# Performance work log

Hardware: AMD Instinct MI355X
Metric: run time of the kernel (lower is better)

## Reference

```python
import jax, jax.numpy as jnp
import numpy as np

# --- static config (matches init_kwargs) ---
B = 2; HI = 60; WI = 60; T = 4; WS = 8; SHIFT = 4
C = 256; NH = 8; HD = C // NH; HID = 1024
P = HI * WI; N = T * P
PAD = (WS - HI % WS) % WS           # 4 -> pad 60 -> 64
HP = HI + PAD; WP = WI + PAD
NWH = HP // WS; NWW = WP // WS
L = WS * WS                          # 64 tokens per window
SCALE = HD ** -0.5

# relative position index [L, L] (constant)
_c = np.stack(np.meshgrid(np.arange(WS), np.arange(WS), indexing='ij')).reshape(2, -1)
_r = (_c[:, :, None] - _c[:, None, :]).transpose(1, 2, 0) + WS - 1
REL_IDX = jnp.asarray(_r[..., 0] * (2 * WS - 1) + _r[..., 1])

# per-window key padding mask [nWin, L] (True = padded token)
_b = np.zeros((HP, WP), bool); _b[HI:, :] = True; _b[:, WI:] = True
WIN_MASK = jnp.asarray(_b.reshape(NWH, WS, NWW, WS).transpose(0, 2, 1, 3).reshape(NWH * NWW, L))


def _ln(x, w, b):
    m = x.mean(-1, keepdims=True)
    v = jnp.square(x - m).mean(-1, keepdims=True)
    return (x - m) * jax.lax.rsqrt(v + 1e-5) * w + b


def _partition(x4):  # [Bm, HP, WP, C] -> [Bm*nWin, L, C]
    Bm = x4.shape[0]
    return x4.reshape(Bm, NWH, WS, NWW, WS, C).transpose(0, 1, 3, 2, 4, 5).reshape(Bm * NWH * NWW, L, C)


def _win_attn(xq, xkv, qw, qb, kw, kb, vw, vb, ow, ob, bias_table):
    Bm = B * T
    q4 = xq.reshape(Bm, HI, WI, C)
    k4 = xkv.reshape(Bm, HI, WI, C)
    q4 = jnp.roll(q4, (-SHIFT, -SHIFT), (1, 2))
    k4 = jnp.roll(k4, (-SHIFT, -SHIFT), (1, 2))
    pad = ((0, 0), (0, PAD), (0, PAD), (0, 0))
    q4 = jnp.pad(q4, pad); k4 = jnp.pad(k4, pad)
    q_win = _partition(q4)   # [Bw, L, C]
    kv_win = _partition(k4)
    q = (q_win @ qw.T + qb).reshape(-1, L, NH, HD)
    k = (kv_win @ kw.T + kb).reshape(-1, L, NH, HD)
    v = (kv_win @ vw.T + vb).reshape(-1, L, NH, HD)
    attn = jnp.einsum('bihd,bjhd->bhij', q, k) * SCALE
    attn = attn + bias_table[REL_IDX].transpose(2, 0, 1)[None]      # RPB [1,H,L,L]
    km = jnp.tile(WIN_MASK, (Bm, 1))                                  # [Bw, L]
    attn = jnp.where(km[:, None, None, :], -jnp.inf, attn)
    p = jax.nn.softmax(attn, axis=-1)
    o = jnp.einsum('bhij,bjhd->bihd', p, v).reshape(-1, L, C)
    o = o @ ow.T + ob
    y = o.reshape(Bm, NWH, NWW, WS, WS, C).transpose(0, 1, 3, 2, 4, 5).reshape(Bm, HP, WP, C)
    y = y[:, :HI, :WI, :]
    y = jnp.roll(y, (SHIFT, SHIFT), (1, 2))
    return y.reshape(B, N, C)


def reference(x, context, ln1_w, ln1_b, ln2_w, ln2_b, ln3_w, ln3_b, lnc_w, lnc_b,
              sa_q_w, sa_q_b, sa_k_w, sa_k_b, sa_v_w, sa_v_b, sa_o_w, sa_o_b, sa_bias,
              ca_q_w, ca_q_b, ca_k_w, ca_k_b, ca_v_w, ca_v_b, ca_o_w, ca_o_b, ca_bias,
              gamma1, gamma2, gamma_mlp, mlp_w1, mlp_b1, mlp_w2, mlp_b2):
    xn = _ln(x, ln1_w, ln1_b)
    y_s = _win_attn(xn, xn, sa_q_w, sa_q_b, sa_k_w, sa_k_b, sa_v_w, sa_v_b, sa_o_w, sa_o_b, sa_bias)
    x = x + gamma1 * y_s
    y_c = _win_attn(_ln(x, ln2_w, ln2_b), _ln(context, lnc_w, lnc_b),
                    ca_q_w, ca_q_b, ca_k_w, ca_k_b, ca_v_w, ca_v_b, ca_o_w, ca_o_b, ca_bias)
    x = x + gamma2 * y_c
    h = _ln(x, ln3_w, ln3_b)
    h = jax.nn.gelu(h @ mlp_w1.T + mlp_b1, approximate=False) @ mlp_w2.T + mlp_b2
    return x + gamma_mlp * h


def setup_inputs() -> dict:
    key = jax.random.key(0)
    ks = jax.random.split(key, 16)
    def w(k, shape, s=0.02):
        return jax.random.normal(k, shape, jnp.float32) * s
    inp = {}
    inp['x'] = jax.random.normal(ks[0], (B, N, C), jnp.float32)
    inp['context'] = jax.random.normal(ks[1], (B, N, C), jnp.float32)
    for nm in ['ln1', 'ln2', 'ln3', 'lnc']:
        inp[f'{nm}_w'] = jnp.ones((C,), jnp.float32)
        inp[f'{nm}_b'] = jnp.zeros((C,), jnp.float32)
    i = 2
    for pfx in ['sa', 'ca']:
        for pn in ['q', 'k', 'v', 'o']:
            inp[f'{pfx}_{pn}_w'] = w(ks[i], (C, C)); i += 1
            inp[f'{pfx}_{pn}_b'] = jnp.zeros((C,), jnp.float32)
        inp[f'{pfx}_bias'] = w(ks[i], ((2 * WS - 1) * (2 * WS - 1), NH)); i += 1
    inp['gamma1'] = jnp.ones((1,), jnp.float32)
    inp['gamma2'] = jnp.ones((1,), jnp.float32)
    inp['gamma_mlp'] = jnp.full((1,), 0.1, jnp.float32)
    inp['mlp_w1'] = w(ks[i], (HID, C)); i += 1
    inp['mlp_b1'] = jnp.zeros((HID,), jnp.float32)
    inp['mlp_w2'] = w(ks[i], (C, HID)); i += 1
    inp['mlp_b2'] = jnp.zeros((C,), jnp.float32)
    return inp
```

## Files before the change

kernel.cpp:

```cpp
#include <hip/hip_runtime.h>
#include <math.h>

#define BN    28800
#define CC    256
#define HIDN  1024
#define WINS  512
#define WROWS (WINS*64)
#define ATT_SCALE 0.1767766952966369f

typedef __bf16 bf16x8 __attribute__((ext_vector_type(8)));
typedef float  f32x4  __attribute__((ext_vector_type(4)));

__device__ __forceinline__ unsigned short f2bf(float f) {
    unsigned u = __float_as_uint(f);
    unsigned r = (u + 0x7FFFu + ((u >> 16) & 1u)) >> 16;
    return (unsigned short)r;
}
__device__ __forceinline__ float bf2f(unsigned short u) {
    return __uint_as_float((unsigned)u << 16);
}

__device__ __forceinline__ float gelu_f(float x) {
    float x3 = x * x * x;
    float e  = __expf(1.5957691216057308f * (x + 0.044715f * x3));
    float th = 1.0f - 2.0f * __builtin_amdgcn_rcpf(e + 1.0f);
    return 0.5f * x * (1.0f + th);
}

__device__ __forceinline__ void gl_lds16(const void* g, void* l) {
    __builtin_amdgcn_global_load_lds(
        (const __attribute__((address_space(1))) void*)g,
        (__attribute__((address_space(3))) void*)l, 16, 0, 0);
}

__global__ void ln_kernel(const float* __restrict__ x, const float* __restrict__ w,
                          const float* __restrict__ b, unsigned short* __restrict__ out, int ntok) {
    int tok  = (int)((blockIdx.x * blockDim.x + threadIdx.x) >> 6);
    int lane = threadIdx.x & 63;
    if (tok >= ntok) return;
    float4 v = reinterpret_cast<const float4*>(x + (size_t)tok * CC)[lane];
    float s  = v.x + v.y + v.z + v.w;
    float s2 = v.x*v.x + v.y*v.y + v.z*v.z + v.w*v.w;
#pragma unroll
    for (int off = 32; off >= 1; off >>= 1) {
        s  += __shfl_xor(s, off);
        s2 += __shfl_xor(s2, off);
    }
    float mean = s * (1.0f / CC);
    float var  = s2 * (1.0f / CC) - mean * mean;
    float rs   = rsqrtf(var + 1e-5f);
    float4 wv = reinterpret_cast<const float4*>(w)[lane];
    float4 bv = reinterpret_cast<const float4*>(b)[lane];
    ushort4 o;
    o.x = f2bf((v.x - mean) * rs * wv.x + bv.x);
    o.y = f2bf((v.y - mean) * rs * wv.y + bv.y);
    o.z = f2bf((v.z - mean) * rs * wv.z + bv.z);
    o.w = f2bf((v.w - mean) * rs * wv.w + bv.w);
    reinterpret_cast<ushort4*>(out + (size_t)tok * CC)[lane] = o;
}

__global__ void ln_gather(const float* __restrict__ x, const float* __restrict__ w,
                          const float* __restrict__ b, unsigned short* __restrict__ dst) {
    int row  = (int)((blockIdx.x * blockDim.x + threadIdx.x) >> 6);
    int lane = threadIdx.x & 63;
    if (row >= WROWS) return;
    int win = row >> 6, l = row & 63;
    int f   = win >> 6;
    int wih = (win >> 3) & 7, wiw = win & 7;
    int r = l >> 3, s = l & 7;
    int h = wih * 8 + r, wc = wiw * 8 + s;
    if (h >= 60 || wc >= 60) {
        ushort4 z = {0, 0, 0, 0};
        reinterpret_cast<ushort4*>(dst + (size_t)row * CC)[lane] = z;
        return;
    }
    int oh = (h + 4) % 60, ow = (wc + 4) % 60;
    size_t tok = (size_t)f * 3600 + (size_t)oh * 60 + ow;
    float4 v = reinterpret_cast<const float4*>(x + tok * CC)[lane];
    float sm  = v.x + v.y + v.z + v.w;
    float s2 = v.x*v.x + v.y*v.y + v.z*v.z + v.w*v.w;
#pragma unroll
    for (int off = 32; off >= 1; off >>= 1) {
        sm += __shfl_xor(sm, off);
        s2 += __shfl_xor(s2, off);
    }
    float mean = sm * (1.0f / CC);
    float var  = s2 * (1.0f / CC) - mean * mean;
    float rs   = rsqrtf(var + 1e-5f);
    float4 wv = reinterpret_cast<const float4*>(w)[lane];
    float4 bv = reinterpret_cast<const float4*>(b)[lane];
    ushort4 o;
    o.x = f2bf((v.x - mean) * rs * wv.x + bv.x);
    o.y = f2bf((v.y - mean) * rs * wv.y + bv.y);
    o.z = f2bf((v.z - mean) * rs * wv.z + bv.z);
    o.w = f2bf((v.w - mean) * rs * wv.w + bv.w);
    reinterpret_cast<ushort4*>(dst + (size_t)row * CC)[lane] = o;
}

template <bool GELU, int FUSE, int TN>
__global__ __launch_bounds__(512, 4) void gemm_wa(
        const unsigned short* __restrict__ Wt,
        const unsigned short* __restrict__ Act,
        const float* __restrict__ b0, const float* __restrict__ b1,
        const float* __restrict__ b2, const float* __restrict__ b3,
        unsigned short* __restrict__ o0, unsigned short* __restrict__ o1,
        unsigned short* __restrict__ o2, unsigned short* __restrict__ o3,
        int strideO, int vseg, int K, int Ntok,
        const float* __restrict__ xres, const float* __restrict__ gammap,
        float* __restrict__ fout) {
    constexpr int NW   = TN / 64;
    constexpr int BP   = TN / 128;
    constexpr int BUFB = 8192 + TN * 64;
    constexpr int POOLB = (3 * BUFB > TN * 256) ? 3 * BUFB : TN * 256;
    __shared__ __align__(16) char pool[POOLB];
    unsigned short* Cs = (unsigned short*)pool;

    const int t = threadIdx.x;
    const int w = t >> 6;
    const int l = t & 63;
    const int Mb = gridDim.x;
    int lin = blockIdx.y * Mb + blockIdx.x;
    int T = Mb * gridDim.y;
    int q = T >> 3, rr = T & 7;
    int xcd = lin & 7, slot = lin >> 3;
    int wid = (xcd < rr) ? (xcd * (q + 1) + slot)
                         : (rr * (q + 1) + (xcd - rr) * q + slot);
    const int m0 = (wid % Mb) * 128;
    const int n0 = (wid / Mb) * TN;

    const int wr = w >> 2, wc = w & 3;
    const int r = l & 15, g = l >> 4;
    const int gp = (g ^ ((r >> 1) & 3)) * 8;
    const int srow = t >> 2;
    const int sgl  = (t & 3) ^ ((srow >> 1) & 3);

    f32x4 acc[4][NW];
#pragma unroll
    for (int i = 0; i < 4; ++i)
#pragma unroll
        for (int j = 0; j < NW; ++j) { acc[i][j][0]=0.f; acc[i][j][1]=0.f; acc[i][j][2]=0.f; acc[i][j][3]=0.f; }

#define STAGE(k0, buf)                                                             \
    do {                                                                           \
        gl_lds16(Wt + (size_t)(m0 + srow) * K + (k0) + sgl * 8,                    \
                 pool + (buf) * BUFB + w * 1024);                                  \
        _Pragma("unroll")                                                          \
        for (int p = 0; p < BP; ++p) {                                             \
            int c    = p * 512 + t;                                                \
            int rowb = c >> 2;                                                     \
            int glb  = (c & 3) ^ ((rowb >> 1) & 3);                                \
            gl_lds16(Act + (size_t)(n0 + rowb) * K + (k0) + glb * 8,               \
                     pool + (buf) * BUFB + 8192 + p * 8192 + w * 1024);            \
        }                                                                          \
    } while (0)

    STAGE(0, 0);
    STAGE(32, 1);
    const char* cb0 = pool;
    const char* cb1 = pool + BUFB;
    const char* cb2 = pool + 2 * BUFB;
    int sbuf = 2;
    const int nt = K >> 5;
    for (int kt = 0; kt < nt; ++kt) {
        if (kt < nt - 1) {
            if (TN == 128) asm volatile("s_waitcnt vmcnt(2)" ::: "memory");
            else           asm volatile("s_waitcnt vmcnt(3)" ::: "memory");
        } else {
            asm volatile("s_waitcnt vmcnt(0)" ::: "memory");
        }
        __builtin_amdgcn_s_barrier();
        __builtin_amdgcn_sched_barrier(0);
        const unsigned short* cA = (const unsigned short*)cb0;
        const unsigned short* cB = (const unsigned short*)(cb0 + 8192);
        bf16x8 bw[NW];
#pragma unroll
        for (int n = 0; n < NW; ++n)
            bw[n] = *reinterpret_cast<const bf16x8*>(&cB[(wc * (NW * 16) + n * 16 + r) * 32 + gp]);
        __builtin_amdgcn_s_setprio(1);
#pragma unroll
        for (int m = 0; m < 4; ++m) {
            bf16x8 af = *reinterpret_cast<const bf16x8*>(&cA[(wr * 64 + m * 16 + r) * 32 + gp]);
#pragma unroll
            for (int n = 0; n < NW; ++n)
                acc[m][n] = __builtin_amdgcn_mfma_f32_16x16x32_bf16(af, bw[n], acc[m][n], 0, 0, 0);
        }
        __builtin_amdgcn_s_setprio(0);
        if (kt + 2 < nt) {
            STAGE((kt + 2) * 32, sbuf);
            sbuf = (sbuf == 2) ? 0 : sbuf + 1;
        }
        const char* tmp = cb0; cb0 = cb1; cb1 = cb2; cb2 = tmp;
    }
#undef STAGE

    const int seg = m0 >> 8;
    const float* bp = (seg == 0) ? b0 : (seg == 1) ? b1 : (seg == 2) ? b2 : b3;
    unsigned short* op = (seg == 0) ? o0 : (seg == 1) ? o1 : (seg == 2) ? o2 : o3;
    const int chseg = m0 & 255;

    if (FUSE == 0 && seg == vseg) {
#pragma unroll
        for (int m = 0; m < 4; ++m) {
            const int ch0 = chseg + wr * 64 + m * 16 + g * 4;
            float4 b4 = *reinterpret_cast<const float4*>(bp + ch0);
            const float bb[4] = {b4.x, b4.y, b4.z, b4.w};
#pragma unroll
            for (int n = 0; n < NW; ++n) {
                const int tok = n0 + wc * (NW * 16) + n * 16 + r;
#pragma unroll
                for (int j = 0; j < 4; ++j)
                    op[(size_t)(ch0 + j) * 32768 + tok] = f2bf(acc[m][n][j] + bb[j]);
            }
        }
        return;
    }

    __syncthreads();
#pragma unroll
    for (int m = 0; m < 4; ++m) {
        const int ch0 = wr * 64 + m * 16 + g * 4;
        float4 b4 = *reinterpret_cast<const float4*>(bp + chseg + ch0);
        const float bb[4] = {b4.x, b4.y, b4.z, b4.w};
#pragma unroll
        for (int n = 0; n < NW; ++n) {
            const int tok_l = wc * (NW * 16) + n * 16 + r;
            float cv[4];
#pragma unroll
            for (int j = 0; j < 4; ++j) {
                cv[j] = acc[m][n][j] + bb[j];
                if (GELU) cv[j] = gelu_f(cv[j]);
            }
            ushort4 pk;
            pk.x = f2bf(cv[0]); pk.y = f2bf(cv[1]); pk.z = f2bf(cv[2]); pk.w = f2bf(cv[3]);
            int gran = (ch0 >> 2) ^ ((tok_l & 15) << 1);
            reinterpret_cast<ushort4*>(Cs)[tok_l * 32 + gran] = pk;
        }
    }
    __syncthreads();
    const int u = t & 15, trow = t >> 4;
    if (FUSE == 0) {
#pragma unroll
        for (int it = 0; it < TN / 32; ++it) {
            int tok_l = it * 32 + trow;
            if (n0 + tok_l >= Ntok) continue;
            int up = u ^ (tok_l & 15);
            uint4 v = reinterpret_cast<const uint4*>(Cs)[tok_l * 16 + up];
            *reinterpret_cast<uint4*>(op + (size_t)(n0 + tok_l) * strideO + chseg + u * 8) = v;
        }
    } else {
        const float gsc = gammap[0];
#pragma unroll
        for (int it = 0; it < TN / 32; ++it) {
            int tok_l = it * 32 + trow;
            int wrow = n0 + tok_l;
            if (wrow >= Ntok) continue;
            int tok;
            if (FUSE == 1) {
                int win = wrow >> 6, l2 = wrow & 63;
                int f = win >> 6, wih = (win >> 3) & 7, wiw = win & 7;
                int r2 = l2 >> 3, s2 = l2 & 7;
                int h = wih * 8 + r2, wcol = wiw * 8 + s2;
                if (h >= 60 || wcol >= 60) continue;
                int oh = h + 4; if (oh >= 60) oh -= 60;
                int ow = wcol + 4; if (ow >= 60) ow -= 60;
                tok = f * 3600 + oh * 60 + ow;
            } else {
                tok = wrow;
            }
            int up = u ^ (tok_l & 15);
            uint4 v = reinterpret_cast<const uint4*>(Cs)[tok_l * 16 + up];
            const unsigned short* pu = (const unsigned short*)&v;
            const float* xr = xres + (size_t)tok * CC + chseg + u * 8;
            float4 xa = *reinterpret_cast<const float4*>(xr);
            float4 xb = *reinterpret_cast<const float4*>(xr + 4);
            float4 oa, ob;
            oa.x = xa.x + gsc * bf2f(pu[0]);
            oa.y = xa.y + gsc * bf2f(pu[1]);
            oa.z = xa.z + gsc * bf2f(pu[2]);
            oa.w = xa.w + gsc * bf2f(pu[3]);
            ob.x = xb.x + gsc * bf2f(pu[4]);
            ob.y = xb.y + gsc * bf2f(pu[5]);
            ob.z = xb.z + gsc * bf2f(pu[6]);
            ob.w = xb.w + gsc * bf2f(pu[7]);
            float* fo = fout + (size_t)tok * CC + chseg + u * 8;
            *reinterpret_cast<float4*>(fo) = oa;
            *reinterpret_cast<float4*>(fo + 4) = ob;
        }
    }
}

__global__ void expand_bias(const float* __restrict__ sa, const float* __restrict__ ca,
                            float* __restrict__ dst) {
    int e = (int)(blockIdx.x * blockDim.x + threadIdx.x);
    const float* src = (e < 16384) ? sa : ca;
    int e2 = e & 16383;
    int h = e2 >> 12, ij = e2 & 4095, i = ij >> 6, j = ij & 63;
    int ri = i >> 3, si = i & 7, rj = j >> 3, sj = j & 7;
    dst[e] = src[((ri - rj + 7) * 15 + (si - sj + 7)) * 8 + h];
}

__global__ __launch_bounds__(256) void attn_mfma(
        const unsigned short* __restrict__ Q,
        const unsigned short* __restrict__ K,
        const unsigned short* __restrict__ VT,
        const float* __restrict__ biasx,
        unsigned short* __restrict__ AO) {
    __shared__ __align__(16) unsigned short Pl[4][64 * 64];
    const int t = threadIdx.x;
    const int w = t >> 6, l = t & 63;
    const int win = blockIdx.x >> 1;
    const int h   = (blockIdx.x & 1) * 4 + w;
    const int c = l & 15, g = l >> 4;
    const int wih = (win >> 3) & 7, wiw = win & 7;
    const size_t qkbase = (size_t)win * 64 * CC + (size_t)h * 32;

    bf16x8 ka[4], qb[4];
#pragma unroll
    for (int mj = 0; mj < 4; ++mj)
        ka[mj] = *reinterpret_cast<const bf16x8*>(K + qkbase + (size_t)(mj * 16 + c) * CC + g * 8);
#pragma unroll
    for (int ni = 0; ni < 4; ++ni)
        qb[ni] = *reinterpret_cast<const bf16x8*>(Q + qkbase + (size_t)(ni * 16 + c) * CC + g * 8);
    f32x4 s[4][4];
#pragma unroll
    for (int mj = 0; mj < 4; ++mj)
#pragma unroll
        for (int ni = 0; ni < 4; ++ni) { s[mj][ni][0]=0.f; s[mj][ni][1]=0.f; s[mj][ni][2]=0.f; s[mj][ni][3]=0.f; }
#pragma unroll
    for (int mj = 0; mj < 4; ++mj)
#pragma unroll
        for (int ni = 0; ni < 4; ++ni)
            s[mj][ni] = __builtin_amdgcn_mfma_f32_16x16x32_bf16(ka[mj], qb[ni], s[mj][ni], 0, 0, 0);

    const float* bx = biasx + h * 4096;
    const bool modd = (wiw == 7) && (g & 1);
#pragma unroll
    for (int mj = 0; mj < 4; ++mj) {
        const bool mmj = (wih == 7) && (mj >= 2);
#pragma unroll
        for (int ni = 0; ni < 4; ++ni) {
            float4 b4 = *reinterpret_cast<const float4*>(bx + (ni * 16 + c) * 64 + mj * 16 + g * 4);
            const float bb[4] = {b4.x, b4.y, b4.z, b4.w};
#pragma unroll
            for (int jj = 0; jj < 4; ++jj) {
                float v = s[mj][ni][jj] * ATT_SCALE + bb[jj];
                s[mj][ni][jj] = (mmj || modd) ? -1e30f : v;
            }
        }
    }

#pragma unroll
    for (int ni = 0; ni < 4; ++ni) {
        float mx = -1e30f;
#pragma unroll
        for (int mj = 0; mj < 4; ++mj)
#pragma unroll
            for (int jj = 0; jj < 4; ++jj) mx = fmaxf(mx, s[mj][ni][jj]);
        mx = fmaxf(mx, __shfl_xor(mx, 16));
        mx = fmaxf(mx, __shfl_xor(mx, 32));
        float sum = 0.f;
#pragma unroll
        for (int mj = 0; mj < 4; ++mj)
#pragma unroll
            for (int jj = 0; jj < 4; ++jj) {
                float p = __expf(s[mj][ni][jj] - mx);
                s[mj][ni][jj] = p;
                sum += p;
            }
        sum += __shfl_xor(sum, 16);
        sum += __shfl_xor(sum, 32);
        float rinv = __builtin_amdgcn_rcpf(sum);
        const int i  = ni * 16 + c;
        const int ik = i & 7;
#pragma unroll
        for (int mj = 0; mj < 4; ++mj) {
            ushort4 pk;
            pk.x = f2bf(s[mj][ni][0] * rinv);
            pk.y = f2bf(s[mj][ni][1] * rinv);
            pk.z = f2bf(s[mj][ni][2] * rinv);
            pk.w = f2bf(s[mj][ni][3] * rinv);
            int chunk = (mj * 2 + (g >> 1)) ^ ik;
            *reinterpret_cast<ushort4*>((char*)&Pl[w][0] + i * 128 + chunk * 16 + (g & 1) * 8) = pk;
        }
    }

    bf16x8 vb[2][2];
#pragma unroll
    for (int nd = 0; nd < 2; ++nd)
#pragma unroll
        for (int kt = 0; kt < 2; ++kt)
            vb[nd][kt] = *reinterpret_cast<const bf16x8*>(
                VT + (size_t)(h * 32 + nd * 16 + c) * 32768 + win * 64 + kt * 32 + g * 8);
    f32x4 o[4][2];
#pragma unroll
    for (int mi = 0; mi < 4; ++mi)
#pragma unroll
        for (int nd = 0; nd < 2; ++nd) { o[mi][nd][0]=0.f; o[mi][nd][1]=0.f; o[mi][nd][2]=0.f; o[mi][nd][3]=0.f; }
#pragma unroll
    for (int mi = 0; mi < 4; ++mi) {
        const int i  = mi * 16 + c;
        const int ik = i & 7;
#pragma unroll
        for (int kt = 0; kt < 2; ++kt) {
            int chunk = (kt * 4 + g) ^ ik;
            bf16x8 pa = *reinterpret_cast<const bf16x8*>((char*)&Pl[w][0] + i * 128 + chunk * 16);
#pragma unroll
            for (int nd = 0; nd < 2; ++nd)
                o[mi][nd] = __builtin_amdgcn_mfma_f32_16x16x32_bf16(pa, vb[nd][kt], o[mi][nd], 0, 0, 0);
        }
    }

    unsigned short* aop = AO + qkbase;
#pragma unroll
    for (int mi = 0; mi < 4; ++mi)
#pragma unroll
        for (int nd = 0; nd < 2; ++nd)
#pragma unroll
            for (int jj = 0; jj < 4; ++jj)
                aop[(size_t)(mi * 16 + g * 4 + jj) * CC + nd * 16 + c] = f2bf(o[mi][nd][jj]);
}

__global__ void cvt_all(const float* s0, const float* s1, const float* s2, const float* s3,
                        const float* s4, const float* s5, const float* s6, const float* s7,
                        const float* s8, const float* s9, unsigned short* __restrict__ dst) {
    const float* srcs[10] = {s0, s1, s2, s3, s4, s5, s6, s7, s8, s9};
    int blk = blockIdx.x;
    int wi = (blk < 512) ? (blk >> 6) : (blk < 768 ? 8 : 9);
    size_t start = (wi < 8) ? (size_t)wi * 65536 : (wi == 8 ? (size_t)524288 : (size_t)786432);
    size_t gidx = (size_t)blk * 1024 + (size_t)threadIdx.x * 4;
    float4 v = *reinterpret_cast<const float4*>(srcs[wi] + (gidx - start));
    ushort4 o;
    o.x = f2bf(v.x); o.y = f2bf(v.y); o.z = f2bf(v.z); o.w = f2bf(v.w);
    *reinterpret_cast<ushort4*>(dst + gidx) = o;
}

extern "C" void kernel_launch(void* const* d_in, const int* in_sizes, int n_in,
                              void* d_out, int out_size, void* d_ws, size_t ws_size,
                              hipStream_t stream) {
    const float* x    = (const float*)d_in[0];
    const float* ctx  = (const float*)d_in[1];
    const float* ln1w = (const float*)d_in[2];
    const float* ln1b = (const float*)d_in[3];
    const float* ln2w = (const float*)d_in[4];
    const float* ln2b = (const float*)d_in[5];
    const float* ln3w = (const float*)d_in[6];
    const float* ln3b = (const float*)d_in[7];
    const float* lncw = (const float*)d_in[8];
    const float* lncb = (const float*)d_in[9];
    const float* saqw = (const float*)d_in[10];
    const float* saqb = (const float*)d_in[11];
    const float* sakw = (const float*)d_in[12];
    const float* sakb = (const float*)d_in[13];
    const float* savw = (const float*)d_in[14];
    const float* savb = (const float*)d_in[15];
    const float* saow = (const float*)d_in[16];
    const float* saob = (const float*)d_in[17];
    const float* sabias = (const float*)d_in[18];
    const float* caqw = (const float*)d_in[19];
    const float* caqb = (const float*)d_in[20];
    const float* cakw = (const float*)d_in[21];
    const float* cakb = (const float*)d_in[22];
    const float* cavw = (const float*)d_in[23];
    const float* cavb = (const float*)d_in[24];
    const float* caow = (const float*)d_in[25];
    const float* caob = (const float*)d_in[26];
    const float* cabias = (const float*)d_in[27];
    const float* gamma1 = (const float*)d_in[28];
    const float* gamma2 = (const float*)d_in[29];
    const float* gammam = (const float*)d_in[30];
    const float* mw1 = (const float*)d_in[31];
    const float* mb1 = (const float*)d_in[32];
    const float* mw2 = (const float*)d_in[33];
    const float* mb2 = (const float*)d_in[34];

    float* ws = (float*)d_ws;
    unsigned short* LNbf = (unsigned short*)(ws);
    unsigned short* Gq   = (unsigned short*)(ws + 3686400);
    unsigned short* Gkv  = (unsigned short*)(ws + 7880704);
    unsigned short* Qbf  = (unsigned short*)(ws + 12075008);
    unsigned short* Kbf  = (unsigned short*)(ws + 16269312);
    unsigned short* VTbf = (unsigned short*)(ws + 20463616);
    float* X1  = ws + 28852224;
    unsigned short* Wp = (unsigned short*)(ws + 36225024);
    float* biasx = ws + 36749312;
    unsigned short* AObf = Gq;
    unsigned short* H1bf = Qbf;

    unsigned short* w_saqkv = Wp;
    unsigned short* w_sao   = Wp + 196608;
    unsigned short* w_caq   = Wp + 262144;
    unsigned short* w_cakv  = Wp + 327680;
    unsigned short* w_cao   = Wp + 458752;
    unsigned short* w_m1    = Wp + 524288;
    unsigned short* w_m2    = Wp + 786432;

    float* OUT = (float*)d_out;

    dim3 blk(256);
    dim3 blk512(512);
    dim3 gLN(BN / 4);
    dim3 gGather(WROWS / 4);
    dim3 gAttn(WINS * 2);

    cvt_all<<<dim3(1024), blk, 0, stream>>>(saqw, sakw, savw, saow, caqw, cakw, cavw, caow, mw1, mw2, Wp);
    expand_bias<<<dim3(128), blk, 0, stream>>>(sabias, cabias, biasx);

    ln_gather<<<gGather, blk, 0, stream>>>(x, ln1w, ln1b, Gq);
    gemm_wa<false,0,256><<<dim3(6, 128), blk512, 0, stream>>>(w_saqkv, Gq, saqb, sakb, savb, savb,
                                                              Qbf, Kbf, VTbf, VTbf, CC, 2, CC, WROWS,
                                                              nullptr, nullptr, nullptr);
    attn_mfma<<<gAttn, blk, 0, stream>>>(Qbf, Kbf, VTbf, biasx, AObf);
    gemm_wa<false,1,128><<<dim3(2, 256), blk512, 0, stream>>>(w_sao, AObf, saob, saob, saob, saob,
                                                              Qbf, Qbf, Qbf, Qbf, CC, -1, CC, WROWS,
                                                              x, gamma1, X1);
    ln_gather<<<gGather, blk, 0, stream>>>(X1, ln2w, ln2b, Gq);
    ln_gather<<<gGather, blk, 0, stream>>>(ctx, lncw, lncb, Gkv);
    gemm_wa<false,0,128><<<dim3(2, 256), blk512, 0, stream>>>(w_caq, Gq, caqb, caqb, caqb, caqb,
                                                              Qbf, Qbf, Qbf, Qbf, CC, -1, CC, WROWS,
                                                              nullptr, nullptr, nullptr);
    gemm_wa<false,0,256><<<dim3(4, 128), blk512, 0, stream>>>(w_cakv, Gkv, cakb, cavb, cavb, cavb,
                                                              Kbf, VTbf, VTbf, VTbf, CC, 1, CC, WROWS,
                                                              nullptr, nullptr, nullptr);
    attn_mfma<<<gAttn, blk, 0, stream>>>(Qbf, Kbf, VTbf, biasx + 16384, AObf);
    gemm_wa<false,1,128><<<dim3(2, 256), blk512, 0, stream>>>(w_cao, AObf, caob, caob, caob, caob,
                                                              Qbf, Qbf, Qbf, Qbf, CC, -1, CC, WROWS,
                                                              X1, gamma2, X1);
    ln_kernel<<<gLN, blk, 0, stream>>>(X1, ln3w, ln3b, LNbf, BN);
    gemm_wa<true,0,256><<<dim3(8, 113), blk512, 0, stream>>>(w_m1, LNbf, mb1, mb1 + 256, mb1 + 512, mb1 + 768,
                                                             H1bf, H1bf + 256, H1bf + 512, H1bf + 768,
                                                             HIDN, -1, CC, BN, nullptr, nullptr, nullptr);
    gemm_wa<false,2,256><<<dim3(2, 113), blk512, 0, stream>>>(w_m2, H1bf, mb2, mb2, mb2, mb2,
                                                             Qbf, Qbf, Qbf, Qbf, CC, -1, HIDN, BN,
                                                             X1, gammam, OUT);
}
```

Baseline: 239.5 us.

## Enlarge GEMM output-channel tile to 256 and stage the epilogue in halves

The weight-activation GEMM now covers 256 output channels per block instead of 128. Each wave accumulates 8x NW MFMA tiles, and twice the weight rows are staged per k-step, so every activation tile loaded from global memory is reused across all channels of a segment. The epilogue writes through LDS in 128-token halves so the C staging buffer fits the pool. Grids are halved in the channel dimension, and the MLP2 GEMM switches to a 128-token tile. The cost is much higher register pressure (launch bounds drop to 2 blocks per SM for TN=256) and larger shared memory, which reduces occupancy.

```diff
diff --git a/kernel.cpp b/kernel.cpp
--- a/kernel.cpp
+++ b/kernel.cpp
@@ -98,7 +98,7 @@
 }
 
 template <bool GELU, int FUSE, int TN>
-__global__ __launch_bounds__(512, 4) void gemm_wa(
+__global__ __launch_bounds__(512, (TN == 128) ? 4 : 2) void gemm_wa(
         const unsigned short* __restrict__ Wt,
         const unsigned short* __restrict__ Act,
         const float* __restrict__ b0, const float* __restrict__ b1,
@@ -110,8 +110,9 @@
         float* __restrict__ fout) {
     constexpr int NW   = TN / 64;
     constexpr int BP   = TN / 128;
-    constexpr int BUFB = 8192 + TN * 64;
-    constexpr int POOLB = (3 * BUFB > TN * 256) ? 3 * BUFB : TN * 256;
+    constexpr int BUFB = 16384 + TN * 64;
+    constexpr int HALVES = TN / 128;
+    constexpr int POOLB = (3 * BUFB > 65536) ? 3 * BUFB : 65536;
     __shared__ __align__(16) char pool[POOLB];
     unsigned short* Cs = (unsigned short*)pool;
 
@@ -125,32 +126,37 @@
     int xcd = lin & 7, slot = lin >> 3;
     int wid = (xcd < rr) ? (xcd * (q + 1) + slot)
                          : (rr * (q + 1) + (xcd - rr) * q + slot);
-    const int m0 = (wid % Mb) * 128;
+    const int m0 = (wid % Mb) * 256;
     const int n0 = (wid / Mb) * TN;
 
-    const int wr = w >> 2, wc = w & 3;
+    const int wr = w >> 2;
+    const int wc = w & 3;
     const int r = l & 15, g = l >> 4;
     const int gp = (g ^ ((r >> 1) & 3)) * 8;
-    const int srow = t >> 2;
-    const int sgl  = (t & 3) ^ ((srow >> 1) & 3);
-
-    f32x4 acc[4][NW];
-#pragma unroll
-    for (int i = 0; i < 4; ++i)
+
+    f32x4 acc[8][NW];
+#pragma unroll
+    for (int i = 0; i < 8; ++i)
 #pragma unroll
         for (int j = 0; j < NW; ++j) { acc[i][j][0]=0.f; acc[i][j][1]=0.f; acc[i][j][2]=0.f; acc[i][j][3]=0.f; }
 
 #define STAGE(k0, buf)                                                             \
     do {                                                                           \
-        gl_lds16(Wt + (size_t)(m0 + srow) * K + (k0) + sgl * 8,                    \
-                 pool + (buf) * BUFB + w * 1024);                                  \
+        _Pragma("unroll")                                                          \
+        for (int p = 0; p < 2; ++p) {                                              \
+            int c    = p * 512 + t;                                                \
+            int rowa = c >> 2;                                                     \
+            int gla  = (c & 3) ^ ((rowa >> 1) & 3);                                \
+            gl_lds16(Wt + (size_t)(m0 + rowa) * K + (k0) + gla * 8,                \
+                     pool + (buf) * BUFB + (p * 512 + w * 64) * 16);               \
+        }                                                                          \
         _Pragma("unroll")                                                          \
         for (int p = 0; p < BP; ++p) {                                             \
             int c    = p * 512 + t;                                                \
             int rowb = c >> 2;                                                     \
             int glb  = (c & 3) ^ ((rowb >> 1) & 3);                                \
             gl_lds16(Act + (size_t)(n0 + rowb) * K + (k0) + glb * 8,               \
-                     pool + (buf) * BUFB + 8192 + p * 8192 + w * 1024);            \
+                     pool + (buf) * BUFB + 16384 + (p * 512 + w * 64) * 16);       \
         }                                                                          \
     } while (0)
 
@@ -163,23 +169,23 @@
     const int nt = K >> 5;
     for (int kt = 0; kt < nt; ++kt) {
         if (kt < nt - 1) {
-            if (TN == 128) asm volatile("s_waitcnt vmcnt(2)" ::: "memory");
-            else           asm volatile("s_waitcnt vmcnt(3)" ::: "memory");
+            if (TN == 128) asm volatile("s_waitcnt vmcnt(3)" ::: "memory");
+            else           asm volatile("s_waitcnt vmcnt(4)" ::: "memory");
         } else {
             asm volatile("s_waitcnt vmcnt(0)" ::: "memory");
         }
         __builtin_amdgcn_s_barrier();
         __builtin_amdgcn_sched_barrier(0);
         const unsigned short* cA = (const unsigned short*)cb0;
-        const unsigned short* cB = (const unsigned short*)(cb0 + 8192);
+        const unsigned short* cB = (const unsigned short*)(cb0 + 16384);
         bf16x8 bw[NW];
 #pragma unroll
         for (int n = 0; n < NW; ++n)
             bw[n] = *reinterpret_cast<const bf16x8*>(&cB[(wc * (NW * 16) + n * 16 + r) * 32 + gp]);
         __builtin_amdgcn_s_setprio(1);
 #pragma unroll
-        for (int m = 0; m < 4; ++m) {
-            bf16x8 af = *reinterpret_cast<const bf16x8*>(&cA[(wr * 64 + m * 16 + r) * 32 + gp]);
+        for (int m = 0; m < 8; ++m) {
+            bf16x8 af = *reinterpret_cast<const bf16x8*>(&cA[(wr * 128 + m * 16 + r) * 32 + gp]);
 #pragma unroll
             for (int n = 0; n < NW; ++n)
                 acc[m][n] = __builtin_amdgcn_mfma_f32_16x16x32_bf16(af, bw[n], acc[m][n], 0, 0, 0);
@@ -196,12 +202,11 @@
     const int seg = m0 >> 8;
     const float* bp = (seg == 0) ? b0 : (seg == 1) ? b1 : (seg == 2) ? b2 : b3;
     unsigned short* op = (seg == 0) ? o0 : (seg == 1) ? o1 : (seg == 2) ? o2 : o3;
-    const int chseg = m0 & 255;
 
     if (FUSE == 0 && seg == vseg) {
 #pragma unroll
-        for (int m = 0; m < 4; ++m) {
-            const int ch0 = chseg + wr * 64 + m * 16 + g * 4;
+        for (int m = 0; m < 8; ++m) {
+            const int ch0 = wr * 128 + m * 16 + g * 4;
             float4 b4 = *reinterpret_cast<const float4*>(bp + ch0);
             const float bb[4] = {b4.x, b4.y, b4.z, b4.w};
 #pragma unroll
@@ -215,76 +220,74 @@
         return;
     }
 
-    __syncthreads();
-#pragma unroll
-    for (int m = 0; m < 4; ++m) {
-        const int ch0 = wr * 64 + m * 16 + g * 4;
-        float4 b4 = *reinterpret_cast<const float4*>(bp + chseg + ch0);
-        const float bb[4] = {b4.x, b4.y, b4.z, b4.w};
-#pragma unroll
-        for (int n = 0; n < NW; ++n) {
-            const int tok_l = wc * (NW * 16) + n * 16 + r;
-            float cv[4];
-#pragma unroll
-            for (int j = 0; j < 4; ++j) {
-                cv[j] = acc[m][n][j] + bb[j];
-                if (GELU) cv[j] = gelu_f(cv[j]);
+    const float gsc = (FUSE != 0) ? gammap[0] : 0.f;
+    const int u16 = t & 31, trow = t >> 5;
+#pragma unroll
+    for (int h = 0; h < HALVES; ++h) {
+        __syncthreads();
+        if (HALVES == 1 || (wc >> 1) == h) {
+#pragma unroll
+            for (int m = 0; m < 8; ++m) {
+                const int ch0 = wr * 128 + m * 16 + g * 4;
+                float4 b4 = *reinterpret_cast<const float4*>(bp + ch0);
+                const float bb[4] = {b4.x, b4.y, b4.z, b4.w};
+#pragma unroll
+                for (int n = 0; n < NW; ++n) {
+                    const int tokh = (wc * (NW * 16) + n * 16 + r) & 127;
+                    float cv[4];
+#pragma unroll
+                    for (int j = 0; j < 4; ++j) {
+                        cv[j] = acc[m][n][j] + bb[j];
+                        if (GELU) cv[j] = gelu_f(cv[j]);
+                    }
+                    ushort4 pk;
+                    pk.x = f2bf(cv[0]); pk.y = f2bf(cv[1]); pk.z = f2bf(cv[2]); pk.w = f2bf(cv[3]);
+                    int gran = (ch0 >> 2) ^ ((tokh & 15) << 1);
+                    reinterpret_cast<ushort4*>(Cs)[tokh * 64 + gran] = pk;
+                }
             }
-            ushort4 pk;
-            pk.x = f2bf(cv[0]); pk.y = f2bf(cv[1]); pk.z = f2bf(cv[2]); pk.w = f2bf(cv[3]);
-            int gran = (ch0 >> 2) ^ ((tok_l & 15) << 1);
-            reinterpret_cast<ushort4*>(Cs)[tok_l * 32 + gran] = pk;
-        }
-    }
-    __syncthreads();
-    const int u = t & 15, trow = t >> 4;
-    if (FUSE == 0) {
-#pragma unroll
-        for (int it = 0; it < TN / 32; ++it) {
-            int tok_l = it * 32 + trow;
-            if (n0 + tok_l >= Ntok) continue;
-            int up = u ^ (tok_l & 15);
-            uint4 v = reinterpret_cast<const uint4*>(Cs)[tok_l * 16 + up];
-            *reinterpret_cast<uint4*>(op + (size_t)(n0 + tok_l) * strideO + chseg + u * 8) = v;
-        }
-    } else {
-        const float gsc = gammap[0];
-#pragma unroll
-        for (int it = 0; it < TN / 32; ++it) {
-            int tok_l = it * 32 + trow;
-            int wrow = n0 + tok_l;
+        }
+        __syncthreads();
+#pragma unroll
+        for (int it = 0; it < 8; ++it) {
+            int rowh = it * 16 + trow;
+            int wrow = n0 + h * 128 + rowh;
             if (wrow >= Ntok) continue;
-            int tok;
-            if (FUSE == 1) {
-                int win = wrow >> 6, l2 = wrow & 63;
-                int f = win >> 6, wih = (win >> 3) & 7, wiw = win & 7;
-                int r2 = l2 >> 3, s2 = l2 & 7;
-                int h = wih * 8 + r2, wcol = wiw * 8 + s2;
-                if (h >= 60 || wcol >= 60) continue;
-                int oh = h + 4; if (oh >= 60) oh -= 60;
-                int ow = wcol + 4; if (ow >= 60) ow -= 60;
-                tok = f * 3600 + oh * 60 + ow;
+            int up = u16 ^ (rowh & 15);
+            uint4 v = reinterpret_cast<const uint4*>(Cs)[rowh * 32 + up];
+            if (FUSE == 0) {
+                *reinterpret_cast<uint4*>(op + (size_t)wrow * strideO + u16 * 8) = v;
             } else {
-                tok = wrow;
+                int tok;
+                if (FUSE == 1) {
+                    int win = wrow >> 6, l2 = wrow & 63;
+                    int f = win >> 6, wih = (win >> 3) & 7, wiw = win & 7;
+                    int r2 = l2 >> 3, s2 = l2 & 7;
+                    int hh = wih * 8 + r2, wcol = wiw * 8 + s2;
+                    if (hh >= 60 || wcol >= 60) continue;
+                    int oh = hh + 4; if (oh >= 60) oh -= 60;
+                    int ow = wcol + 4; if (ow >= 60) ow -= 60;
+                    tok = f * 3600 + oh * 60 + ow;
+                } else {
+                    tok = wrow;
+                }
+                const unsigned short* pu = (const unsigned short*)&v;
+                const float* xr = xres + (size_t)tok * CC + u16 * 8;
+                float4 xa = *reinterpret_cast<const float4*>(xr);
+                float4 xb = *reinterpret_cast<const float4*>(xr + 4);
+                float4 oa, ob;
+                oa.x = xa.x + gsc * bf2f(pu[0]);
+                oa.y = xa.y + gsc * bf2f(pu[1]);
+                oa.z = xa.z + gsc * bf2f(pu[2]);
+                oa.w = xa.w + gsc * bf2f(pu[3]);
+                ob.x = xb.x + gsc * bf2f(pu[4]);
+                ob.y = xb.y + gsc * bf2f(pu[5]);
+                ob.z = xb.z + gsc * bf2f(pu[6]);
+                ob.w = xb.w + gsc * bf2f(pu[7]);
+                float* fo = fout + (size_t)tok * CC + u16 * 8;
+                *reinterpret_cast<float4*>(fo) = oa;
+                *reinterpret_cast<float4*>(fo + 4) = ob;
             }
-            int up = u ^ (tok_l & 15);
-            uint4 v = reinterpret_cast<const uint4*>(Cs)[tok_l * 16 + up];
-            const unsigned short* pu = (const unsigned short*)&v;
-            const float* xr = xres + (size_t)tok * CC + chseg + u * 8;
-            float4 xa = *reinterpret_cast<const float4*>(xr);
-            float4 xb = *reinterpret_cast<const float4*>(xr + 4);
-            float4 oa, ob;
-            oa.x = xa.x + gsc * bf2f(pu[0]);
-            oa.y = xa.y + gsc * bf2f(pu[1]);
-            oa.z = xa.z + gsc * bf2f(pu[2]);
-            oa.w = xa.w + gsc * bf2f(pu[3]);
-            ob.x = xb.x + gsc * bf2f(pu[4]);
-            ob.y = xb.y + gsc * bf2f(pu[5]);
-            ob.z = xb.z + gsc * bf2f(pu[6]);
-            ob.w = xb.w + gsc * bf2f(pu[7]);
-            float* fo = fout + (size_t)tok * CC + chseg + u * 8;
-            *reinterpret_cast<float4*>(fo) = oa;
-            *reinterpret_cast<float4*>(fo + 4) = ob;
         }
     }
 }
@@ -506,30 +509,30 @@
     expand_bias<<<dim3(128), blk, 0, stream>>>(sabias, cabias, biasx);
 
     ln_gather<<<gGather, blk, 0, stream>>>(x, ln1w, ln1b, Gq);
-    gemm_wa<false,0,256><<<dim3(6, 128), blk512, 0, stream>>>(w_saqkv, Gq, saqb, sakb, savb, savb,
+    gemm_wa<false,0,256><<<dim3(3, 128), blk512, 0, stream>>>(w_saqkv, Gq, saqb, sakb, savb, savb,
                                                               Qbf, Kbf, VTbf, VTbf, CC, 2, CC, WROWS,
                                                               nullptr, nullptr, nullptr);
     attn_mfma<<<gAttn, blk, 0, stream>>>(Qbf, Kbf, VTbf, biasx, AObf);
-    gemm_wa<false,1,128><<<dim3(2, 256), blk512, 0, stream>>>(w_sao, AObf, saob, saob, saob, saob,
+    gemm_wa<false,1,128><<<dim3(1, 256), blk512, 0, stream>>>(w_sao, AObf, saob, saob, saob, saob,
                                                               Qbf, Qbf, Qbf, Qbf, CC, -1, CC, WROWS,
                                                               x, gamma1, X1);
     ln_gather<<<gGather, blk, 0, stream>>>(X1, ln2w, ln2b, Gq);
     ln_gather<<<gGather, blk, 0, stream>>>(ctx, lncw, lncb, Gkv);
-    gemm_wa<false,0,128><<<dim3(2, 256), blk512, 0, stream>>>(w_caq, Gq, caqb, caqb, caqb, caqb,
+    gemm_wa<false,0,128><<<dim3(1, 256), blk512, 0, stream>>>(w_caq, Gq, caqb, caqb, caqb, caqb,
                                                               Qbf, Qbf, Qbf, Qbf, CC, -1, CC, WROWS,
                                                               nullptr, nullptr, nullptr);
-    gemm_wa<false,0,256><<<dim3(4, 128), blk512, 0, stream>>>(w_cakv, Gkv, cakb, cavb, cavb, cavb,
+    gemm_wa<false,0,256><<<dim3(2, 128), blk512, 0, stream>>>(w_cakv, Gkv, cakb, cavb, cavb, cavb,
                                                               Kbf, VTbf, VTbf, VTbf, CC, 1, CC, WROWS,
                                                               nullptr, nullptr, nullptr);
     attn_mfma<<<gAttn, blk, 0, stream>>>(Qbf, Kbf, VTbf, biasx + 16384, AObf);
-    gemm_wa<false,1,128><<<dim3(2, 256), blk512, 0, stream>>>(w_cao, AObf, caob, caob, caob, caob,
+    gemm_wa<false,1,128><<<dim3(1, 256), blk512, 0, stream>>>(w_cao, AObf, caob, caob, caob, caob,
                                                               Qbf, Qbf, Qbf, Qbf, CC, -1, CC, WROWS,
                                                               X1, gamma2, X1);
     ln_kernel<<<gLN, blk, 0, stream>>>(X1, ln3w, ln3b, LNbf, BN);
-    gemm_wa<true,0,256><<<dim3(8, 113), blk512, 0, stream>>>(w_m1, LNbf, mb1, mb1 + 256, mb1 + 512, mb1 + 768,
+    gemm_wa<true,0,256><<<dim3(4, 113), blk512, 0, stream>>>(w_m1, LNbf, mb1, mb1 + 256, mb1 + 512, mb1 + 768,
                                                              H1bf, H1bf + 256, H1bf + 512, H1bf + 768,
                                                              HIDN, -1, CC, BN, nullptr, nullptr, nullptr);
-    gemm_wa<false,2,256><<<dim3(2, 113), blk512, 0, stream>>>(w_m2, H1bf, mb2, mb2, mb2, mb2,
+    gemm_wa<false,2,128><<<dim3(1, 225), blk512, 0, stream>>>(w_m2, H1bf, mb2, mb2, mb2, mb2,
                                                              Qbf, Qbf, Qbf, Qbf, CC, -1, HIDN, BN,
                                                              X1, gammam, OUT);
 }
```

Measured after the change: 263.9 us. +10.2%, slower.

## Fuse output projection, residual add and following LayerNorm into one GEMM kernel

Applied to the files above, without the earlier changes.

Adds a gemm_ln kernel that computes the full 256-channel output projection per 128-token tile, so each block holds whole rows and can apply the residual add and the next LayerNorm in its epilogue. This replaces the separate ln_gather after self-attention and the ln_kernel after cross-attention, removing a full re-read of the fp32 residual stream and two launches. The cost is a larger per-block tile with fewer blocks (256), which may lower parallelism. AObf is moved to its own buffer so the fused kernel can write Gq while reading the attention output.

```diff
diff --git a/kernel.cpp b/kernel.cpp
--- a/kernel.cpp
+++ b/kernel.cpp
@@ -31,32 +31,6 @@
     __builtin_amdgcn_global_load_lds(
         (const __attribute__((address_space(1))) void*)g,
         (__attribute__((address_space(3))) void*)l, 16, 0, 0);
-}
-
-__global__ void ln_kernel(const float* __restrict__ x, const float* __restrict__ w,
-                          const float* __restrict__ b, unsigned short* __restrict__ out, int ntok) {
-    int tok  = (int)((blockIdx.x * blockDim.x + threadIdx.x) >> 6);
-    int lane = threadIdx.x & 63;
-    if (tok >= ntok) return;
-    float4 v = reinterpret_cast<const float4*>(x + (size_t)tok * CC)[lane];
-    float s  = v.x + v.y + v.z + v.w;
-    float s2 = v.x*v.x + v.y*v.y + v.z*v.z + v.w*v.w;
-#pragma unroll
-    for (int off = 32; off >= 1; off >>= 1) {
-        s  += __shfl_xor(s, off);
-        s2 += __shfl_xor(s2, off);
-    }
-    float mean = s * (1.0f / CC);
-    float var  = s2 * (1.0f / CC) - mean * mean;
-    float rs   = rsqrtf(var + 1e-5f);
-    float4 wv = reinterpret_cast<const float4*>(w)[lane];
-    float4 bv = reinterpret_cast<const float4*>(b)[lane];
-    ushort4 o;
-    o.x = f2bf((v.x - mean) * rs * wv.x + bv.x);
-    o.y = f2bf((v.y - mean) * rs * wv.y + bv.y);
-    o.z = f2bf((v.z - mean) * rs * wv.z + bv.z);
-    o.w = f2bf((v.w - mean) * rs * wv.w + bv.w);
-    reinterpret_cast<ushort4*>(out + (size_t)tok * CC)[lane] = o;
 }
 
 __global__ void ln_gather(const float* __restrict__ x, const float* __restrict__ w,
@@ -254,19 +228,7 @@
             int tok_l = it * 32 + trow;
             int wrow = n0 + tok_l;
             if (wrow >= Ntok) continue;
-            int tok;
-            if (FUSE == 1) {
-                int win = wrow >> 6, l2 = wrow & 63;
-                int f = win >> 6, wih = (win >> 3) & 7, wiw = win & 7;
-                int r2 = l2 >> 3, s2 = l2 & 7;
-                int h = wih * 8 + r2, wcol = wiw * 8 + s2;
-                if (h >= 60 || wcol >= 60) continue;
-                int oh = h + 4; if (oh >= 60) oh -= 60;
-                int ow = wcol + 4; if (ow >= 60) ow -= 60;
-                tok = f * 3600 + oh * 60 + ow;
-            } else {
-                tok = wrow;
-            }
+            int tok = wrow;
             int up = u ^ (tok_l & 15);
             uint4 v = reinterpret_cast<const uint4*>(Cs)[tok_l * 16 + up];
             const unsigned short* pu = (const unsigned short*)&v;
@@ -286,6 +248,181 @@
             *reinterpret_cast<float4*>(fo) = oa;
             *reinterpret_cast<float4*>(fo + 4) = ob;
         }
+    }
+}
+
+template <int LNM>
+__global__ __launch_bounds__(512, 4) void gemm_ln(
+        const unsigned short* __restrict__ Wt,
+        const unsigned short* __restrict__ Act,
+        const float* __restrict__ bias,
+        const float* __restrict__ xres, const float* __restrict__ gammap,
+        float* __restrict__ fout,
+        const float* __restrict__ lnw, const float* __restrict__ lnb,
+        unsigned short* __restrict__ lnout) {
+    constexpr int BUFB = 16384 + 8192;
+    __shared__ __align__(16) char pool[3 * BUFB];
+    unsigned short* Cs = (unsigned short*)pool;
+
+    const int t = threadIdx.x, w = t >> 6, l = t & 63;
+    int lin = blockIdx.x;
+    int T = gridDim.x;
+    int q = T >> 3, rr = T & 7;
+    int xcd = lin & 7, slot = lin >> 3;
+    int wid = (xcd < rr) ? (xcd * (q + 1) + slot)
+                         : (rr * (q + 1) + (xcd - rr) * q + slot);
+    const int n0 = wid * 128;
+
+    const int wr = w >> 2, wc = w & 3;
+    const int r = l & 15, g = l >> 4;
+    const int gp = (g ^ ((r >> 1) & 3)) * 8;
+    const int K = 256;
+
+    f32x4 acc[8][2];
+#pragma unroll
+    for (int i = 0; i < 8; ++i)
+#pragma unroll
+        for (int j = 0; j < 2; ++j) { acc[i][j][0]=0.f; acc[i][j][1]=0.f; acc[i][j][2]=0.f; acc[i][j][3]=0.f; }
+
+#define STAGE(k0, buf)                                                             \
+    do {                                                                           \
+        _Pragma("unroll")                                                          \
+        for (int p = 0; p < 2; ++p) {                                              \
+            int c    = p * 512 + t;                                                \
+            int rowa = c >> 2;                                                     \
+            int gla  = (c & 3) ^ ((rowa >> 1) & 3);                                \
+            gl_lds16(Wt + (size_t)rowa * K + (k0) + gla * 8,                       \
+                     pool + (buf) * BUFB + (p * 512 + w * 64) * 16);               \
+        }                                                                          \
+        {                                                                          \
+            int rowb = t >> 2;                                                     \
+            int glb  = (t & 3) ^ ((rowb >> 1) & 3);                                \
+            gl_lds16(Act + (size_t)(n0 + rowb) * K + (k0) + glb * 8,               \
+                     pool + (buf) * BUFB + 16384 + w * 1024);                      \
+        }                                                                          \
+    } while (0)
+
+    STAGE(0, 0);
+    STAGE(32, 1);
+    const char* cb0 = pool;
+    const char* cb1 = pool + BUFB;
+    const char* cb2 = pool + 2 * BUFB;
+    int sbuf = 2;
+    for (int kt = 0; kt < 8; ++kt) {
+        if (kt < 7) asm volatile("s_waitcnt vmcnt(3)" ::: "memory");
+        else        asm volatile("s_waitcnt vmcnt(0)" ::: "memory");
+        __builtin_amdgcn_s_barrier();
+        __builtin_amdgcn_sched_barrier(0);
+        const unsigned short* cA = (const unsigned short*)cb0;
+        const unsigned short* cB = (const unsigned short*)(cb0 + 16384);
+        bf16x8 bw[2];
+#pragma unroll
+        for (int n = 0; n < 2; ++n)
+            bw[n] = *reinterpret_cast<const bf16x8*>(&cB[(wc * 32 + n * 16 + r) * 32 + gp]);
+        __builtin_amdgcn_s_setprio(1);
+#pragma unroll
+        for (int m = 0; m < 8; ++m) {
+            bf16x8 af = *reinterpret_cast<const bf16x8*>(&cA[(wr * 128 + m * 16 + r) * 32 + gp]);
+#pragma unroll
+            for (int n = 0; n < 2; ++n)
+                acc[m][n] = __builtin_amdgcn_mfma_f32_16x16x32_bf16(af, bw[n], acc[m][n], 0, 0, 0);
+        }
+        __builtin_amdgcn_s_setprio(0);
+        if (kt + 2 < 8) {
+            STAGE((kt + 2) * 32, sbuf);
+            sbuf = (sbuf == 2) ? 0 : sbuf + 1;
+        }
+        const char* tmp = cb0; cb0 = cb1; cb1 = cb2; cb2 = tmp;
+    }
+#undef STAGE
+
+    __syncthreads();
+#pragma unroll
+    for (int m = 0; m < 8; ++m) {
+        const int ch0 = wr * 128 + m * 16 + g * 4;
+        float4 b4 = *reinterpret_cast<const float4*>(bias + ch0);
+        const float bb[4] = {b4.x, b4.y, b4.z, b4.w};
+#pragma unroll
+        for (int n = 0; n < 2; ++n) {
+            const int tokh = wc * 32 + n * 16 + r;
+            ushort4 pk;
+            pk.x = f2bf(acc[m][n][0] + bb[0]);
+            pk.y = f2bf(acc[m][n][1] + bb[1]);
+            pk.z = f2bf(acc[m][n][2] + bb[2]);
+            pk.w = f2bf(acc[m][n][3] + bb[3]);
+            int gran = (ch0 >> 2) ^ ((tokh & 15) << 1);
+            reinterpret_cast<ushort4*>(Cs)[tokh * 64 + gran] = pk;
+        }
+    }
+    __syncthreads();
+
+    const float gsc = gammap[0];
+    const int u16 = t & 31, trow = t >> 5;
+#pragma unroll
+    for (int it = 0; it < 8; ++it) {
+        int rowh = it * 16 + trow;
+        int wrow = n0 + rowh;
+        int win = wrow >> 6, l2 = wrow & 63;
+        int f = win >> 6, wih = (win >> 3) & 7, wiw = win & 7;
+        int r2 = l2 >> 3, s2 = l2 & 7;
+        int hh = wih * 8 + r2, wcol = wiw * 8 + s2;
+        bool pad = (hh >= 60) || (wcol >= 60);
+        if (pad) {
+            if (LNM == 1) {
+                uint4 z = {0u, 0u, 0u, 0u};
+                *reinterpret_cast<uint4*>(lnout + (size_t)wrow * CC + u16 * 8) = z;
+            }
+            continue;
+        }
+        int oh = hh + 4; if (oh >= 60) oh -= 60;
+        int ow = wcol + 4; if (ow >= 60) ow -= 60;
+        int tok = f * 3600 + oh * 60 + ow;
+
+        int up = u16 ^ (rowh & 15);
+        uint4 v = reinterpret_cast<const uint4*>(Cs)[rowh * 32 + up];
+        const unsigned short* pu = (const unsigned short*)&v;
+        const float* xr = xres + (size_t)tok * CC + u16 * 8;
+        float4 xa = *reinterpret_cast<const float4*>(xr);
+        float4 xb = *reinterpret_cast<const float4*>(xr + 4);
+        float4 oa, ob;
+        oa.x = xa.x + gsc * bf2f(pu[0]);
+        oa.y = xa.y + gsc * bf2f(pu[1]);
+        oa.z = xa.z + gsc * bf2f(pu[2]);
+        oa.w = xa.w + gsc * bf2f(pu[3]);
+        ob.x = xb.x + gsc * bf2f(pu[4]);
+        ob.y = xb.y + gsc * bf2f(pu[5]);
+        ob.z = xb.z + gsc * bf2f(pu[6]);
+        ob.w = xb.w + gsc * bf2f(pu[7]);
+        float* fo = fout + (size_t)tok * CC + u16 * 8;
+        *reinterpret_cast<float4*>(fo) = oa;
+        *reinterpret_cast<float4*>(fo + 4) = ob;
+
+        float sm = oa.x + oa.y + oa.z + oa.w + ob.x + ob.y + ob.z + ob.w;
+        float s2q = oa.x*oa.x + oa.y*oa.y + oa.z*oa.z + oa.w*oa.w
+                  + ob.x*ob.x + ob.y*ob.y + ob.z*ob.z + ob.w*ob.w;
+#pragma unroll
+        for (int off = 1; off <= 16; off <<= 1) {
+            sm  += __shfl_xor(sm, off);
+            s2q += __shfl_xor(s2q, off);
+        }
+        float mean = sm * (1.0f / CC);
+        float rs   = rsqrtf(s2q * (1.0f / CC) - mean * mean + 1e-5f);
+        float4 w0 = *reinterpret_cast<const float4*>(lnw + u16 * 8);
+        float4 w1 = *reinterpret_cast<const float4*>(lnw + u16 * 8 + 4);
+        float4 c0 = *reinterpret_cast<const float4*>(lnb + u16 * 8);
+        float4 c1 = *reinterpret_cast<const float4*>(lnb + u16 * 8 + 4);
+        ushort4 pa, pb;
+        pa.x = f2bf((oa.x - mean) * rs * w0.x + c0.x);
+        pa.y = f2bf((oa.y - mean) * rs * w0.y + c0.y);
+        pa.z = f2bf((oa.z - mean) * rs * w0.z + c0.z);
+        pa.w = f2bf((oa.w - mean) * rs * w0.w + c0.w);
+        pb.x = f2bf((ob.x - mean) * rs * w1.x + c1.x);
+        pb.y = f2bf((ob.y - mean) * rs * w1.y + c1.y);
+        pb.z = f2bf((ob.z - mean) * rs * w1.z + c1.z);
+        pb.w = f2bf((ob.w - mean) * rs * w1.w + c1.w);
+        size_t dst = (size_t)((LNM == 1) ? wrow : tok) * CC + u16 * 8;
+        *reinterpret_cast<ushort4*>(lnout + dst)     = pa;
+        *reinterpret_cast<ushort4*>(lnout + dst + 4) = pb;
     }
 }
 
@@ -480,10 +617,10 @@
     unsigned short* Qbf  = (unsigned short*)(ws + 12075008);
     unsigned short* Kbf  = (unsigned short*)(ws + 16269312);
     unsigned short* VTbf = (unsigned short*)(ws + 20463616);
+    unsigned short* AObf = (unsigned short*)(ws + 24657920);
     float* X1  = ws + 28852224;
     unsigned short* Wp = (unsigned short*)(ws + 36225024);
     float* biasx = ws + 36749312;
-    unsigned short* AObf = Gq;
     unsigned short* H1bf = Qbf;
 
     unsigned short* w_saqkv = Wp;
@@ -498,7 +635,6 @@
 
     dim3 blk(256);
     dim3 blk512(512);
-    dim3 gLN(BN / 4);
     dim3 gGather(WROWS / 4);
     dim3 gAttn(WINS * 2);
 
@@ -510,10 +646,8 @@
                                                               Qbf, Kbf, VTbf, VTbf, CC, 2, CC, WROWS,
                                                               nullptr, nullptr, nullptr);
     attn_mfma<<<gAttn, blk, 0, stream>>>(Qbf, Kbf, VTbf, biasx, AObf);
-    gemm_wa<false,1,128><<<dim3(2, 256), blk512, 0, stream>>>(w_sao, AObf, saob, saob, saob, saob,
-                                                              Qbf, Qbf, Qbf, Qbf, CC, -1, CC, WROWS,
-                                                              x, gamma1, X1);
-    ln_gather<<<gGather, blk, 0, stream>>>(X1, ln2w, ln2b, Gq);
+    gemm_ln<1><<<dim3(256), blk512, 0, stream>>>(w_sao, AObf, saob, x, gamma1, X1, ln2w, ln2b, Gq);
+
     ln_gather<<<gGather, blk, 0, stream>>>(ctx, lncw, lncb, Gkv);
     gemm_wa<false,0,128><<<dim3(2, 256), blk512, 0, stream>>>(w_caq, Gq, caqb, caqb, caqb, caqb,
                                                               Qbf, Qbf, Qbf, Qbf, CC, -1, CC, WROWS,
@@ -522,10 +656,8 @@
                                                               Kbf, VTbf, VTbf, VTbf, CC, 1, CC, WROWS,
                                                               nullptr, nullptr, nullptr);
     attn_mfma<<<gAttn, blk, 0, stream>>>(Qbf, Kbf, VTbf, biasx + 16384, AObf);
-    gemm_wa<false,1,128><<<dim3(2, 256), blk512, 0, stream>>>(w_cao, AObf, caob, caob, caob, caob,
-                                                              Qbf, Qbf, Qbf, Qbf, CC, -1, CC, WROWS,
-                                                              X1, gamma2, X1);
-    ln_kernel<<<gLN, blk, 0, stream>>>(X1, ln3w, ln3b, LNbf, BN);
+    gemm_ln<2><<<dim3(256), blk512, 0, stream>>>(w_cao, AObf, caob, X1, gamma2, X1, ln3w, ln3b, LNbf);
+
     gemm_wa<true,0,256><<<dim3(8, 113), blk512, 0, stream>>>(w_m1, LNbf, mb1, mb1 + 256, mb1 + 512, mb1 + 768,
                                                              H1bf, H1bf + 256, H1bf + 512, H1bf + 768,
                                                              HIDN, -1, CC, BN, nullptr, nullptr, nullptr);
```

Measured after the change: 225.1 us. -6.0%, faster.
